# Kernel optimization log

Measured on AMD Instinct MI355X. Metric: run time of the kernel, lower is better.

The kernel has to match this reference:

```python
import jax, jax.numpy as jnp
import numpy as np

# ---- config (from cfg / InstantNGP defaults) ----
W_IMG, H_IMG = 1024, 1024            # uv_reso_w, uv_reso_h
N_LEVELS = 16                        # standard InstantNGP level count
BASE_RES = 16
FINEST_RES = 1024                    # cfg['finest_level']
F_FEAT = 2                           # features per level
LOG2_T = 19                          # cfg['log2_hashmap_size']
T = 1 << LOG2_T
HIDDEN = 64
PRIMES = np.array([1, 2654435761], dtype=np.uint32)  # 2D spatial-hash primes


def setup_inputs() -> dict:
    key = jax.random.key(0)
    ks = jax.random.split(key, 5)
    d_in = N_LEVELS * F_FEAT
    tables = jax.random.uniform(ks[0], (N_LEVELS, T, F_FEAT), jnp.float32, -1e-4, 1e-4)
    W1 = jax.random.normal(ks[1], (d_in, HIDDEN), jnp.float32) / np.sqrt(d_in)
    b1 = jnp.zeros((HIDDEN,), jnp.float32)
    W2 = jax.random.normal(ks[2], (HIDDEN, HIDDEN), jnp.float32) / np.sqrt(HIDDEN)
    b2 = jnp.zeros((HIDDEN,), jnp.float32)
    W3 = jax.random.normal(ks[3], (HIDDEN, 3), jnp.float32) / np.sqrt(HIDDEN)
    b3 = jnp.zeros((3,), jnp.float32)
    return {"tables": tables, "W1": W1, "b1": b1, "W2": W2, "b2": b2, "W3": W3, "b3": b3}


def _uv_coords():
    # replicate torch.meshgrid(arange(W), arange(H), indexing='xy') -> (H, W)
    xx, yy = jnp.meshgrid(jnp.arange(W_IMG), jnp.arange(H_IMG), indexing='xy')
    x = xx.ravel().astype(jnp.float32) / W_IMG
    y = yy.ravel().astype(jnp.float32) / H_IMG
    return jnp.stack([x, y], axis=1)  # [N, 2]


def _hash_encode(coord, tables):
    # coord: [N,2] in [0,1); tables: [L,T,F]
    growth = np.exp((np.log(FINEST_RES) - np.log(BASE_RES)) / (N_LEVELS - 1))
    res = np.floor(BASE_RES * growth ** np.arange(N_LEVELS)).astype(np.float32)  # [L]
    scaled = coord[None, :, :] * res[:, None, None]          # [L,N,2]
    c0f = jnp.floor(scaled)
    frac = scaled - c0f                                       # [L,N,2]
    c0 = c0f.astype(jnp.uint32)
    corners = jnp.array([[0, 0], [1, 0], [0, 1], [1, 1]], dtype=jnp.uint32)  # [4,2]
    cc = c0[:, :, None, :] + corners[None, None]              # [L,N,4,2]
    idx = (cc[..., 0] * jnp.uint32(PRIMES[0])) ^ (cc[..., 1] * jnp.uint32(PRIMES[1]))
    idx = (idx & jnp.uint32(T - 1)).astype(jnp.int32)         # [L,N,4]
    feats = jax.vmap(lambda tab, i: tab[i])(tables, idx)      # [L,N,4,F] scattered gather
    cf = corners.astype(jnp.float32)                          # [4,2]
    # bilinear weights: prod over dims of (frac if corner bit else 1-frac)
    w = jnp.prod(cf[None, None] * frac[:, :, None, :] +
                 (1.0 - cf[None, None]) * (1.0 - frac[:, :, None, :]), axis=-1)  # [L,N,4]
    feat = jnp.einsum('lnc,lncf->lnf', w, feats)              # [L,N,F]
    return jnp.transpose(feat, (1, 0, 2)).reshape(-1, N_LEVELS * F_FEAT)  # [N, L*F]


def reference(tables, W1, b1, W2, b2, W3, b3):
    coord = _uv_coords()                                      # [N,2]
    enc = _hash_encode(coord, tables)                         # [N,32]
    h = jax.nn.relu(enc @ W1 + b1)
    h = jax.nn.relu(h @ W2 + b2)
    out = h @ W3 + b3                                         # [N,3]
    img = out.reshape(H_IMG, W_IMG, 3).transpose(2, 0, 1)     # [3,H,W]
    return jax.nn.sigmoid(img)[None, ...]                     # [1,3,H,W]
```

## Files before the change

kernel.cpp:

```cpp
#include <hip/hip_runtime.h>
#include <math.h>

#define NLEV   16
#define TSIZE  524288
#define TMASK  524287
#define NPIX   (1024*1024)

typedef __attribute__((ext_vector_type(8))) short s8v;
typedef __attribute__((ext_vector_type(4))) float f4v;

struct ResArr { float r[NLEV]; };
union Frag { unsigned int u[4]; s8v v; };

__device__ __forceinline__ unsigned short bf16_rn(float x) {
    unsigned int u = __builtin_bit_cast(unsigned int, x);
    u += 0x7fffu + ((u >> 16) & 1u);
    return (unsigned short)(u >> 16);
}
__device__ __forceinline__ unsigned int pk_bf16(float lo, float hi) {
    return __builtin_amdgcn_perm(__builtin_bit_cast(unsigned int, hi),
                                 __builtin_bit_cast(unsigned int, lo),
                                 0x07060302u);
}

__global__ __launch_bounds__(256) void prep_kernel(
    const float* __restrict__ W1, const float* __restrict__ W2,
    const float* __restrict__ W3, float* __restrict__ ws, ResArr res)
{
    const int t = threadIdx.x;
    if (t < NLEV) ws[t] = res.r[t];
    unsigned short* w1t = (unsigned short*)(ws + 16);
    unsigned short* w2t = w1t + 64 * 32;
    unsigned short* w3t = w2t + 64 * 64;
    for (int i = t; i < 64 * 32; i += 256) {
        int n = i >> 5, k = i & 31;
        w1t[i] = bf16_rn(W1[k * 64 + n]);
    }
    for (int i = t; i < 64 * 64; i += 256) {
        int n2 = i >> 6, kp = i & 63;
        int klog = (kp & 32) | ((kp & 4) << 2) | ((kp & 24) >> 1) | (kp & 3);
        w2t[i] = bf16_rn(W2[klog * 64 + n2]);
    }
    for (int i = t; i < 16 * 64; i += 256) {
        int row = i >> 6, kp = i & 63;
        int klog = (kp & 32) | ((kp & 4) << 2) | ((kp & 24) >> 1) | (kp & 3);
        int ch = row & 3;
        w3t[i] = (ch < 3) ? bf16_rn(W3[klog * 3 + ch]) : (unsigned short)0;
    }
}

#define NCORN 221

__global__ __launch_bounds__(256) void ngp_fused_kernel(
    const float* __restrict__ tables,
    const float* __restrict__ b1, const float* __restrict__ b2,
    const float* __restrict__ b3,
    const float* __restrict__ ws, float* __restrict__ out)
{
    __shared__ float2 ldsc[NCORN];

    const int tid  = threadIdx.x;
    const int lane = tid & 63;
    const int wv   = tid >> 6;
    const int c15  = lane & 15;
    const int g    = lane >> 4;
    const int xb   = blockIdx.x * 16;
    const int yb   = blockIdx.y * 16;

    constexpr int WCL[12]  = {3,3,3,3,3,3,4,4,5,5,6,7};
    constexpr int OFFL[12] = {0,9,18,27,36,45,54,70,86,111,136,172};

    const float xbf = (float)xb * (1.0f / 1024.0f);
    const float ybf = (float)yb * (1.0f / 1024.0f);

    if (tid < NCORN) {
        #pragma unroll
        for (int l = 0; l < 12; ++l) {
            const int sz = WCL[l] * WCL[l];
            if (tid >= OFFL[l] && tid < OFFL[l] + sz) {
                const int local = tid - OFFL[l];
                const int jj = local / WCL[l];
                const int ii = local - jj * WCL[l];
                const float r = ws[l];
                const int cx0 = (int)floorf(xbf * r);
                const int cy0 = (int)floorf(ybf * r);
                const unsigned int idx =
                    (((unsigned int)(cx0 + ii)) ^
                     ((unsigned int)(cy0 + jj) * 2654435761u)) & TMASK;
                ldsc[tid] = ((const float2*)tables)[(size_t)l * TSIZE + idx];
            }
        }
    }
    __syncthreads();

    const float4 rv = *(const float4*)(ws + g * 4);
    const float rr[4] = { rv.x, rv.y, rv.z, rv.w };
    const float xs = (float)(xb + c15) * (1.0f / 1024.0f);
    float yf[4];
    #pragma unroll
    for (int pt = 0; pt < 4; ++pt)
        yf[pt] = (float)(yb + wv * 4 + pt) * (1.0f / 1024.0f);

    Frag bfrag[4];

    if (g < 3) {
        #pragma unroll
        for (int j = 0; j < 4; ++j) {
            const int lWc  = (g == 0) ? WCL[j]  : (g == 1) ? WCL[4 + j]  : WCL[8 + j];
            const int lOff = (g == 0) ? OFFL[j] : (g == 1) ? OFFL[4 + j] : OFFL[8 + j];
            const float r   = rr[j];
            const float sx  = xs * r;
            const float fx0 = floorf(sx);
            const float fx  = sx - fx0;
            const int ii    = (int)fx0 - (int)floorf(xbf * r);
            const int cy0i  = (int)floorf(ybf * r);
            #pragma unroll
            for (int pt = 0; pt < 4; ++pt) {
                const float sy  = yf[pt] * r;
                const float fy0 = floorf(sy);
                const float fy  = sy - fy0;
                const int jj    = (int)fy0 - cy0i;
                const int base  = lOff + jj * lWc + ii;
                const float2 c00 = ldsc[base];
                const float2 c10 = ldsc[base + 1];
                const float2 c01 = ldsc[base + lWc];
                const float2 c11 = ldsc[base + lWc + 1];
                const float w00 = (1.0f - fx) * (1.0f - fy);
                const float w10 = fx          * (1.0f - fy);
                const float w01 = (1.0f - fx) * fy;
                const float w11 = fx          * fy;
                bfrag[pt].u[j] = pk_bf16(
                    w00 * c00.x + w10 * c10.x + w01 * c01.x + w11 * c11.x,
                    w00 * c00.y + w10 * c10.y + w01 * c01.y + w11 * c11.y);
            }
        }
    } else {
        #pragma unroll
        for (int j = 0; j < 4; ++j) {
            const float r   = rr[j];
            const float sx  = xs * r;
            const float fx0 = floorf(sx);
            const float fx  = sx - fx0;
            const unsigned int cx  = (unsigned int)fx0;
            const unsigned int cx1 = cx + 1u;
            const float2* __restrict__ tab =
                (const float2*)tables + (size_t)(12 + j) * TSIZE;
            #pragma unroll
            for (int pt = 0; pt < 4; ++pt) {
                const float sy  = yf[pt] * r;
                const float fy0 = floorf(sy);
                const float fy  = sy - fy0;
                const unsigned int cy  = (unsigned int)fy0;
                const unsigned int hy0 = cy * 2654435761u;
                const unsigned int hy1 = hy0 + 2654435761u;
                const float2 f00 = tab[(cx  ^ hy0) & TMASK];
                const float2 f10 = tab[(cx1 ^ hy0) & TMASK];
                const float2 f01 = tab[(cx  ^ hy1) & TMASK];
                const float2 f11 = tab[(cx1 ^ hy1) & TMASK];
                const float w00 = (1.0f - fx) * (1.0f - fy);
                const float w10 = fx          * (1.0f - fy);
                const float w01 = (1.0f - fx) * fy;
                const float w11 = fx          * fy;
                bfrag[pt].u[j] = pk_bf16(
                    w00 * f00.x + w10 * f10.x + w01 * f01.x + w11 * f11.x,
                    w00 * f00.y + w10 * f10.y + w01 * f01.y + w11 * f11.y);
            }
        }
    }

    const unsigned short* __restrict__ w1t = (const unsigned short*)(ws + 16);
    const unsigned short* __restrict__ w2t = w1t + 64 * 32;
    const unsigned short* __restrict__ w3t = w2t + 64 * 64;

    unsigned int hp[4][4][2];
    #pragma unroll
    for (int mt = 0; mt < 4; ++mt) {
        Frag afr;
        afr.v = *(const s8v*)(w1t + (mt * 16 + c15) * 32 + g * 8);
        const float4 bb = *(const float4*)(b1 + mt * 16 + g * 4);
        #pragma unroll
        for (int pt = 0; pt < 4; ++pt) {
            f4v acc = (f4v){0.f, 0.f, 0.f, 0.f};
            acc = __builtin_amdgcn_mfma_f32_16x16x32_bf16(
                afr.v, bfrag[pt].v, acc, 0, 0, 0);
            const float v0 = fmaxf(acc[0] + bb.x, 0.0f);
            const float v1 = fmaxf(acc[1] + bb.y, 0.0f);
            const float v2 = fmaxf(acc[2] + bb.z, 0.0f);
            const float v3 = fmaxf(acc[3] + bb.w, 0.0f);
            hp[mt][pt][0] = pk_bf16(v0, v1);
            hp[mt][pt][1] = pk_bf16(v2, v3);
        }
    }

    unsigned int hq[4][4][2];
    #pragma unroll
    for (int mt = 0; mt < 4; ++mt) {
        const float4 bb2 = *(const float4*)(b2 + mt * 16 + g * 4);
        f4v acc[4];
        #pragma unroll
        for (int pt = 0; pt < 4; ++pt) acc[pt] = (f4v){0.f, 0.f, 0.f, 0.f};
        #pragma unroll
        for (int st = 0; st < 2; ++st) {
            Frag a2, bf2[4];
            a2.v = *(const s8v*)(w2t + (mt * 16 + c15) * 64 + st * 32 + g * 8);
            #pragma unroll
            for (int pt = 0; pt < 4; ++pt) {
                bf2[pt].u[0] = hp[2 * st + 0][pt][0];
                bf2[pt].u[1] = hp[2 * st + 0][pt][1];
                bf2[pt].u[2] = hp[2 * st + 1][pt][0];
                bf2[pt].u[3] = hp[2 * st + 1][pt][1];
            }
            #pragma unroll
            for (int pt = 0; pt < 4; ++pt)
                acc[pt] = __builtin_amdgcn_mfma_f32_16x16x32_bf16(
                    a2.v, bf2[pt].v, acc[pt], 0, 0, 0);
        }
        #pragma unroll
        for (int pt = 0; pt < 4; ++pt) {
            const float v0 = fmaxf(acc[pt][0] + bb2.x, 0.0f);
            const float v1 = fmaxf(acc[pt][1] + bb2.y, 0.0f);
            const float v2 = fmaxf(acc[pt][2] + bb2.z, 0.0f);
            const float v3 = fmaxf(acc[pt][3] + bb2.w, 0.0f);
            hq[mt][pt][0] = pk_bf16(v0, v1);
            hq[mt][pt][1] = pk_bf16(v2, v3);
        }
    }

    f4v acc3[4];
    #pragma unroll
    for (int pt = 0; pt < 4; ++pt) acc3[pt] = (f4v){0.f, 0.f, 0.f, 0.f};
    #pragma unroll
    for (int st = 0; st < 2; ++st) {
        Frag a3, bf3[4];
        a3.v = *(const s8v*)(w3t + c15 * 64 + st * 32 + g * 8);
        #pragma unroll
        for (int pt = 0; pt < 4; ++pt) {
            bf3[pt].u[0] = hq[2 * st + 0][pt][0];
            bf3[pt].u[1] = hq[2 * st + 0][pt][1];
            bf3[pt].u[2] = hq[2 * st + 1][pt][0];
            bf3[pt].u[3] = hq[2 * st + 1][pt][1];
        }
        #pragma unroll
        for (int pt = 0; pt < 4; ++pt)
            acc3[pt] = __builtin_amdgcn_mfma_f32_16x16x32_bf16(
                a3.v, bf3[pt].v, acc3[pt], 0, 0, 0);
    }

    float ov[3];
    #pragma unroll
    for (int c = 0; c < 3; ++c) {
        float v = acc3[0][c];
        v = (g == 1) ? acc3[1][c] : v;
        v = (g == 2) ? acc3[2][c] : v;
        v = (g == 3) ? acc3[3][c] : v;
        ov[c] = v + b3[c];
    }
    const int pix = ((yb + wv * 4 + g) << 10) + xb + c15;
    out[0 * NPIX + pix] = 1.0f / (1.0f + __expf(-ov[0]));
    out[1 * NPIX + pix] = 1.0f / (1.0f + __expf(-ov[1]));
    out[2 * NPIX + pix] = 1.0f / (1.0f + __expf(-ov[2]));
}

extern "C" void kernel_launch(void* const* d_in, const int* in_sizes, int n_in,
                              void* d_out, int out_size, void* d_ws, size_t ws_size,
                              hipStream_t stream) {
    const float* tables = (const float*)d_in[0];
    const float* W1     = (const float*)d_in[1];
    const float* b1     = (const float*)d_in[2];
    const float* W2     = (const float*)d_in[3];
    const float* b2     = (const float*)d_in[4];
    const float* W3     = (const float*)d_in[5];
    const float* b3     = (const float*)d_in[6];
    float* out          = (float*)d_out;
    float* ws           = (float*)d_ws;

    ResArr res;
    const double growth = exp((log(1024.0) - log(16.0)) / 15.0);
    for (int l = 0; l < NLEV; ++l)
        res.r[l] = (float)floor(16.0 * pow(growth, (double)l));

    hipLaunchKernelGGL(prep_kernel, dim3(1), dim3(256), 0, stream, W1, W2, W3, ws, res);
    hipLaunchKernelGGL(ngp_fused_kernel, dim3(64, 64), dim3(256), 0, stream,
                       tables, b1, b2, b3, ws, out);
}
```

Measured before the change: 77.29 us.

## Stage fine-level hash corners in LDS and gather coarse levels directly

The per-block LDS staging of corner features moves from the 12 coarse levels to the three fine levels 12-14, which have 9x9, 11x11 and 14x14 corner windows per 16x16 tile. The coarse levels 0-11 are now gathered straight from global memory, where they should hit in cache because their tables are small in practice. The finest level (res 1024) has zero fractional offset on this pixel grid, so it is sampled with a single fetch instead of four. This cuts scattered global gathers on the fine levels, which have poor locality, in exchange for a larger LDS fill and per-thread global loads on the coarse levels.

```diff
diff --git a/kernel.cpp b/kernel.cpp
--- a/kernel.cpp
+++ b/kernel.cpp
@@ -49,7 +49,7 @@
     }
 }
 
-#define NCORN 221
+#define NFC 398
 
 __global__ __launch_bounds__(256) void ngp_fused_kernel(
     const float* __restrict__ tables,
@@ -57,7 +57,7 @@
     const float* __restrict__ b3,
     const float* __restrict__ ws, float* __restrict__ out)
 {
-    __shared__ float2 ldsc[NCORN];
+    __shared__ float2 ldsf[NFC];
 
     const int tid  = threadIdx.x;
     const int lane = tid & 63;
@@ -67,29 +67,23 @@
     const int xb   = blockIdx.x * 16;
     const int yb   = blockIdx.y * 16;
 
-    constexpr int WCL[12]  = {3,3,3,3,3,3,4,4,5,5,6,7};
-    constexpr int OFFL[12] = {0,9,18,27,36,45,54,70,86,111,136,172};
-
     const float xbf = (float)xb * (1.0f / 1024.0f);
     const float ybf = (float)yb * (1.0f / 1024.0f);
 
-    if (tid < NCORN) {
-        #pragma unroll
-        for (int l = 0; l < 12; ++l) {
-            const int sz = WCL[l] * WCL[l];
-            if (tid >= OFFL[l] && tid < OFFL[l] + sz) {
-                const int local = tid - OFFL[l];
-                const int jj = local / WCL[l];
-                const int ii = local - jj * WCL[l];
-                const float r = ws[l];
-                const int cx0 = (int)floorf(xbf * r);
-                const int cy0 = (int)floorf(ybf * r);
-                const unsigned int idx =
-                    (((unsigned int)(cx0 + ii)) ^
-                     ((unsigned int)(cy0 + jj) * 2654435761u)) & TMASK;
-                ldsc[tid] = ((const float2*)tables)[(size_t)l * TSIZE + idx];
-            }
-        }
+    for (int i = tid; i < NFC; i += 256) {
+        int l, loc, wc;
+        if (i < 81)       { l = 0; loc = i;       wc = 9;  }
+        else if (i < 202) { l = 1; loc = i - 81;  wc = 11; }
+        else              { l = 2; loc = i - 202; wc = 14; }
+        const int jj = loc / wc;
+        const int ii = loc - jj * wc;
+        const float r = ws[12 + l];
+        const int cx0 = (int)floorf(xbf * r);
+        const int cy0 = (int)floorf(ybf * r);
+        const unsigned int idx =
+            (((unsigned int)(cx0 + ii)) ^
+             ((unsigned int)(cy0 + jj) * 2654435761u)) & TMASK;
+        ldsf[i] = ((const float2*)tables)[(size_t)(12 + l) * TSIZE + idx];
     }
     __syncthreads();
 
@@ -104,37 +98,6 @@
     Frag bfrag[4];
 
     if (g < 3) {
-        #pragma unroll
-        for (int j = 0; j < 4; ++j) {
-            const int lWc  = (g == 0) ? WCL[j]  : (g == 1) ? WCL[4 + j]  : WCL[8 + j];
-            const int lOff = (g == 0) ? OFFL[j] : (g == 1) ? OFFL[4 + j] : OFFL[8 + j];
-            const float r   = rr[j];
-            const float sx  = xs * r;
-            const float fx0 = floorf(sx);
-            const float fx  = sx - fx0;
-            const int ii    = (int)fx0 - (int)floorf(xbf * r);
-            const int cy0i  = (int)floorf(ybf * r);
-            #pragma unroll
-            for (int pt = 0; pt < 4; ++pt) {
-                const float sy  = yf[pt] * r;
-                const float fy0 = floorf(sy);
-                const float fy  = sy - fy0;
-                const int jj    = (int)fy0 - cy0i;
-                const int base  = lOff + jj * lWc + ii;
-                const float2 c00 = ldsc[base];
-                const float2 c10 = ldsc[base + 1];
-                const float2 c01 = ldsc[base + lWc];
-                const float2 c11 = ldsc[base + lWc + 1];
-                const float w00 = (1.0f - fx) * (1.0f - fy);
-                const float w10 = fx          * (1.0f - fy);
-                const float w01 = (1.0f - fx) * fy;
-                const float w11 = fx          * fy;
-                bfrag[pt].u[j] = pk_bf16(
-                    w00 * c00.x + w10 * c10.x + w01 * c01.x + w11 * c11.x,
-                    w00 * c00.y + w10 * c10.y + w01 * c01.y + w11 * c11.y);
-            }
-        }
-    } else {
         #pragma unroll
         for (int j = 0; j < 4; ++j) {
             const float r   = rr[j];
@@ -144,7 +107,7 @@
             const unsigned int cx  = (unsigned int)fx0;
             const unsigned int cx1 = cx + 1u;
             const float2* __restrict__ tab =
-                (const float2*)tables + (size_t)(12 + j) * TSIZE;
+                (const float2*)tables + (size_t)(g * 4 + j) * TSIZE;
             #pragma unroll
             for (int pt = 0; pt < 4; ++pt) {
                 const float sy  = yf[pt] * r;
@@ -166,6 +129,50 @@
                     w00 * f00.y + w10 * f10.y + w01 * f01.y + w11 * f11.y);
             }
         }
+    } else {
+        const int FWC[3]  = {9, 11, 14};
+        const int FOFF[3] = {0, 81, 202};
+        #pragma unroll
+        for (int j = 0; j < 3; ++j) {
+            const int wc  = FWC[j];
+            const int off = FOFF[j];
+            const float r   = rr[j];
+            const float sx  = xs * r;
+            const float fx0 = floorf(sx);
+            const float fx  = sx - fx0;
+            const int ii    = (int)fx0 - (int)floorf(xbf * r);
+            const int cy0i  = (int)floorf(ybf * r);
+            #pragma unroll
+            for (int pt = 0; pt < 4; ++pt) {
+                const float sy  = yf[pt] * r;
+                const float fy0 = floorf(sy);
+                const float fy  = sy - fy0;
+                const int jj    = (int)fy0 - cy0i;
+                const int base  = off + jj * wc + ii;
+                const float2 c00 = ldsf[base];
+                const float2 c10 = ldsf[base + 1];
+                const float2 c01 = ldsf[base + wc];
+                const float2 c11 = ldsf[base + wc + 1];
+                const float w00 = (1.0f - fx) * (1.0f - fy);
+                const float w10 = fx          * (1.0f - fy);
+                const float w01 = (1.0f - fx) * fy;
+                const float w11 = fx          * fy;
+                bfrag[pt].u[j] = pk_bf16(
+                    w00 * c00.x + w10 * c10.x + w01 * c01.x + w11 * c11.x,
+                    w00 * c00.y + w10 * c10.y + w01 * c01.y + w11 * c11.y);
+            }
+        }
+        {
+            const float2* __restrict__ tab =
+                (const float2*)tables + (size_t)15 * TSIZE;
+            const unsigned int cx = (unsigned int)(xb + c15);
+            #pragma unroll
+            for (int pt = 0; pt < 4; ++pt) {
+                const unsigned int cy = (unsigned int)(yb + wv * 4 + pt);
+                const float2 f00 = tab[(cx ^ (cy * 2654435761u)) & TMASK];
+                bfrag[pt].u[3] = pk_bf16(f00.x, f00.y);
+            }
+        }
     }
 
     const unsigned short* __restrict__ w1t = (const unsigned short*)(ws + 16);
```

After: 73.54 us. 4.9% less time.
